# Kernel tuning notes

Hardware: AMD Instinct MI355X
Metric: run time of the kernel (lower is better)

## Reference

```python
import jax, jax.numpy as jnp
import numpy as np

LMAX = 2
C1 = 64; C2 = 64; COUT = 64
B = 4096
SUM_RDIM = sum(3**L for L in range(LMAX + 1))   # 13
FEAT1 = C1 * SUM_RDIM                            # 832
FEAT2 = C2 * SUM_RDIM


def _enumerate_paths(Lmax):
    paths = []
    for L1 in range(Lmax + 1):
        for L2 in range(Lmax + 1):
            for k in range(min(L1, L2) + 1):
                Lout = L1 + L2 - 2 * k
                if 0 <= Lout <= Lmax:
                    paths.append((L1, L2, Lout, k, False))
            if L1 >= 1 and L2 >= 1:
                for k in range(min(L1 - 1, L2 - 1) + 1):
                    Lout = L1 + L2 - 2 * k - 1
                    if 0 <= Lout <= Lmax:
                        paths.append((L1, L2, Lout, k, True))
    return paths

PATHS = _enumerate_paths(LMAX)   # 15 paths for Lmax=2


def _path_eq(L1, L2, k, use_eps):
    # Fused equation: W[c,a,b] contracted together with the delta/eps path einsum.
    letters = list('defghijklmnopqrstuvwxyz')  # a,b,c reserved for channels
    i_idx = letters[:L1]
    j_idx = letters[L1:L1 + L2]
    for r in range(k):  # delta: contract last k indices of A with last k of B
        j_idx[L2 - k + r] = i_idx[L1 - k + r]
    i_free = i_idx[:L1 - k]
    j_free = j_idx[:L2 - k]
    eps_sub = None
    if use_eps:  # consume last free index of each side via eps_{p i j}
        p = letters[L1 + L2]
        eps_sub = p + i_free[-1] + j_free[-1]
        i_free, j_free = i_free[:-1], j_free[:-1]
        out = i_free + j_free + [p]
    else:
        out = i_free + j_free
    terms = ['cab', '...a' + ''.join(i_idx), '...b' + ''.join(j_idx)]
    if eps_sub is not None:
        terms.append(eps_sub)
    return ','.join(terms) + '->...c' + ''.join(out)


def _epsilon():
    e = np.zeros((3, 3, 3), dtype=np.float32)
    e[0, 1, 2] = e[1, 2, 0] = e[2, 0, 1] = 1.0
    e[2, 1, 0] = e[1, 0, 2] = e[0, 2, 1] = -1.0
    return jnp.asarray(e)


def _split_by_rank(x, C, Lmax):
    batch = x.shape[:-1]
    out, idx = {}, 0
    for L in range(Lmax + 1):
        d = C * 3**L
        blk = x[..., idx:idx + d]
        idx += d
        out[L] = blk.reshape(*batch, C) if L == 0 else blk.reshape(*batch, C, *((3,) * L))
    return out


def setup_inputs() -> dict:
    key = jax.random.key(0)
    k1, k2, k3 = jax.random.split(key, 3)
    x1 = jax.random.normal(k1, (B, FEAT1), dtype=jnp.float32)
    x2 = jax.random.normal(k2, (B, FEAT2), dtype=jnp.float32)
    weight = jax.random.normal(k3, (len(PATHS) * COUT * C1 * C2,), dtype=jnp.float32) * 0.02
    return {"x1": x1, "x2": x2, "weight": weight}


def reference(x1, x2, weight):
    A = _split_by_rank(x1, C1, LMAX)
    Bt = _split_by_rank(x2, C2, LMAX)
    eps = _epsilon().astype(x1.dtype)
    batch = x1.shape[:-1]
    blocks = {L: jnp.zeros((*batch, COUT) + (3,) * L, dtype=x1.dtype) for L in range(LMAX + 1)}
    wsz = COUT * C1 * C2
    for n, (L1, L2, Lout, k, use_eps) in enumerate(PATHS):
        Wp = weight[n * wsz:(n + 1) * wsz].reshape(COUT, C1, C2)
        eq = _path_eq(L1, L2, k, use_eps)
        ops = (Wp, A[L1], Bt[L2]) + ((eps,) if use_eps else ())
        blocks[Lout] = blocks[Lout] + jnp.einsum(eq, *ops, optimize='optimal')
    parts = [blocks[L].reshape(*batch, COUT * 3**L) for L in range(LMAX + 1)]
    return jnp.concatenate(parts, axis=-1)
```

## Files before the change

kernel.cpp:

```cpp
#include <hip/hip_runtime.h>
#include <cstdint>
#include <cstddef>


#define FEAT 832
#define ZT 64

typedef _Float16 half8 __attribute__((ext_vector_type(8)));
typedef float floatx16 __attribute__((ext_vector_type(16)));

struct Chunk {
  int wbase;
  int o1[3];
  int o2[3];
  float sg[3];
  int d1, d2, nt;
};

__global__ void swz_w_kernel(const float* __restrict__ w, _Float16* __restrict__ o) {
  const int i = blockIdx.x * 256 + threadIdx.x;
  const int lane = i & 63;
  const int pkc  = i >> 6;
  const int cgrp = pkc & 1;
  const int ksg  = (pkc >> 1) & 255;
  const int p    = pkc >> 9;
  const int c  = cgrp * 32 + (lane & 31);
  const int k0 = ksg * 16 + (lane >> 5) * 8;
  const float* src = w + (size_t)p * 262144 + (size_t)c * 4096 + k0;
  const float4 v0 = *(const float4*)(src);
  const float4 v1 = *(const float4*)(src + 4);
  half8 h = { (_Float16)v0.x, (_Float16)v0.y, (_Float16)v0.z, (_Float16)v0.w,
              (_Float16)v1.x, (_Float16)v1.y, (_Float16)v1.z, (_Float16)v1.w };
  *(half8*)(o + (size_t)i * 8) = h;
}

__global__ __launch_bounds__(256) void gather_kernel(
    float* __restrict__ out, const float* __restrict__ part, int np)
{
  __shared__ float T[64][65];
  const int zb = blockIdx.x * 64;
  const int fb = blockIdx.y * 64;
  const int tid = threadIdx.x;
  const int fl = tid >> 6;
  const int zl = tid & 63;
  #pragma unroll
  for (int i = 0; i < 16; ++i) {
    const int f = fb + fl + i * 4;
    int s, c;
    if (f < 64)       { s = 0;              c = f; }
    else if (f < 256) { const int g = f - 64;  c = g / 3; s = 1 + g % 3; }
    else              { const int g = f - 256; c = g / 9; s = 4 + g % 9; }
    const size_t base = (size_t)s * 262144 + (size_t)c * 4096 + zb + zl;
    float v = 0.0f;
    for (int q = 0; q < np; ++q)
      v += part[(size_t)q * 3407872 + base];
    T[fl + i * 4][zl] = v;
  }
  __syncthreads();
  const int zr = tid >> 6;
  const int fc = tid & 63;
  #pragma unroll
  for (int i = 0; i < 16; ++i) {
    const int z = zr + i * 4;
    float* o = out + (size_t)(zb + z) * FEAT + fb + fc;
    *o += T[fc][z];
  }
}

__device__ __forceinline__ half8 splat8(_Float16 h) {
  return half8{h, h, h, h, h, h, h, h};
}

template<int NT>
__device__ __forceinline__ void run_chunk(
    const Chunk C, const int zbase, const int zl, const int hf,
    const int lane, const int tid,
    const float* __restrict__ x1, const float* __restrict__ x2,
    const _Float16* __restrict__ Wh,
    _Float16* __restrict__ XS2, _Float16* __restrict__ XS1,
    floatx16& acc0, floatx16& acc1)
{
  __syncthreads();

  #pragma unroll
  for (int t = 0; t < NT; ++t) {
    const size_t base2 = (size_t)zbase * FEAT + C.o2[t];
    for (int e = tid; e < 4096; e += 128) {
      const int zz = e >> 6, b = e & 63;
      XS2[(t * 64 + zz) * 72 + b] =
          (_Float16)x2[base2 + (size_t)zz * FEAT + b * C.d2];
    }
  }
  #pragma unroll
  for (int t = 0; t < NT; ++t) {
    const float sgf = C.sg[t];
    const int o1 = C.o1[t];
    for (int e = tid; e < 4096; e += 128) {
      const int a = e & 63, zz = e >> 6;
      XS1[(t * 64 + a) * 66 + zz] =
          (_Float16)(x1[(size_t)(zbase + zz) * FEAT + o1 + a * C.d1] * sgf);
    }
  }
  __syncthreads();

  half8 x2r[NT][4];
  #pragma unroll
  for (int t = 0; t < NT; ++t) {
    #pragma unroll
    for (int ks = 0; ks < 4; ++ks)
      x2r[t][ks] = *(const half8*)&XS2[(t * 64 + zl) * 72 + ks * 16 + hf * 8];
  }

  const _Float16* __restrict__ Wq = Wh + C.wbase + lane * 8;
  const _Float16* __restrict__ Xq = XS1 + zl;

  half8 afE[2][4], afO[2][4];
  #pragma unroll
  for (int ks = 0; ks < 4; ++ks) {
    afE[0][ks] = *(const half8*)(Wq + ks * 1024);
    afE[1][ks] = *(const half8*)(Wq + ks * 1024 + 512);
    afO[0][ks] = *(const half8*)(Wq + 4096 + ks * 1024);
    afO[1][ks] = *(const half8*)(Wq + 4096 + ks * 1024 + 512);
  }
  _Float16 sc[NT], scn[NT];
  #pragma unroll
  for (int t = 0; t < NT; ++t) {
    sc[t]  = Xq[(t * 64 + 0) * 66];
    scn[t] = Xq[(t * 64 + 1) * 66];
  }

  #pragma unroll 1
  for (int a = 0; a < 64; a += 2) {
    {
      half8 sv[NT];
      #pragma unroll
      for (int t = 0; t < NT; ++t) sv[t] = splat8(sc[t]);
      if (a + 2 < 64) {
        #pragma unroll
        for (int t = 0; t < NT; ++t) sc[t] = Xq[(t * 64 + a + 2) * 66];
      }
      #pragma unroll
      for (int ks = 0; ks < 4; ++ks) {
        half8 tb = sv[0] * x2r[0][ks];
        if (NT > 1) tb += sv[1] * x2r[1][ks];
        if (NT > 2) tb += sv[2] * x2r[2][ks];
        acc0 = __builtin_amdgcn_mfma_f32_32x32x16_f16(afE[0][ks], tb, acc0, 0, 0, 0);
        acc1 = __builtin_amdgcn_mfma_f32_32x32x16_f16(afE[1][ks], tb, acc1, 0, 0, 0);
      }
      if (a + 2 < 64) {
        const _Float16* wn = Wq + (a + 2) * 4096;
        #pragma unroll
        for (int ks = 0; ks < 4; ++ks) {
          afE[0][ks] = *(const half8*)(wn + ks * 1024);
          afE[1][ks] = *(const half8*)(wn + ks * 1024 + 512);
        }
      }
    }
    {
      half8 sv[NT];
      #pragma unroll
      for (int t = 0; t < NT; ++t) sv[t] = splat8(scn[t]);
      if (a + 3 < 64) {
        #pragma unroll
        for (int t = 0; t < NT; ++t) scn[t] = Xq[(t * 64 + a + 3) * 66];
      }
      #pragma unroll
      for (int ks = 0; ks < 4; ++ks) {
        half8 tb = sv[0] * x2r[0][ks];
        if (NT > 1) tb += sv[1] * x2r[1][ks];
        if (NT > 2) tb += sv[2] * x2r[2][ks];
        acc0 = __builtin_amdgcn_mfma_f32_32x32x16_f16(afO[0][ks], tb, acc0, 0, 0, 0);
        acc1 = __builtin_amdgcn_mfma_f32_32x32x16_f16(afO[1][ks], tb, acc1, 0, 0, 0);
      }
      if (a + 3 < 64) {
        const _Float16* wn = Wq + (a + 3) * 4096;
        #pragma unroll
        for (int ks = 0; ks < 4; ++ks) {
          afO[0][ks] = *(const half8*)(wn + ks * 1024);
          afO[1][ks] = *(const half8*)(wn + ks * 1024 + 512);
        }
      }
    }
  }
}

__global__ __launch_bounds__(128, 2) void tp_kernel(
    const float* __restrict__ x1, const float* __restrict__ x2,
    const _Float16* __restrict__ Wh, float* __restrict__ out,
    float* __restrict__ part)
{
  __shared__ __align__(16) _Float16 XS2[3 * 64 * 72];
  __shared__ __align__(16) _Float16 XS1[3 * 64 * 66];
  __shared__ Chunk chs[7];
  __shared__ int nch_s;

  const int tid  = threadIdx.x;
  const int slot = blockIdx.y;
  const int q    = blockIdx.z;
  const int nsplit = gridDim.z;
  const int zbase = blockIdx.x * ZT;
  const int zgrp = tid >> 6;
  const int lane = tid & 63;
  const int ln31 = lane & 31;
  const int hf   = lane >> 5;
  const int zl   = zgrp * 32 + ln31;

  int offO, dO, mO;
  if (slot == 0)      { offO = 0;   dO = 1; mO = 0; }
  else if (slot < 4)  { offO = 64;  dO = 3; mO = slot - 1; }
  else                { offO = 256; dO = 9; mO = slot - 4; }

  if (tid == 0) {
    int n = 0;
    auto add = [&](int p, int L1, int L2,
                   int i0, int i1, int i2, int j0, int j1, int j2,
                   float s0, float s1, float s2, int nt) {
      const int offs[3] = {0, 64, 256};
      const int ds[3]   = {1, 3, 9};
      Chunk c;
      c.wbase = p * 262144;
      c.o1[0] = offs[L1] + i0; c.o1[1] = offs[L1] + i1; c.o1[2] = offs[L1] + i2;
      c.o2[0] = offs[L2] + j0; c.o2[1] = offs[L2] + j1; c.o2[2] = offs[L2] + j2;
      c.sg[0] = s0; c.sg[1] = s1; c.sg[2] = s2;
      c.d1 = ds[L1]; c.d2 = ds[L2]; c.nt = nt;
      chs[n++] = c;
    };
    if (slot == 0) {
      add(0, 0,0, 0,0,0, 0,0,0, 1,0,0, 1);
      add(5, 1,1, 0,1,2, 0,1,2, 1,1,1, 3);
      add(13,2,2, 0,1,2, 0,1,2, 1,1,1, 3);
      add(13,2,2, 3,4,5, 3,4,5, 1,1,1, 3);
      add(13,2,2, 6,7,8, 6,7,8, 1,1,1, 3);
    } else if (slot < 4) {
      const int m = slot - 1, p1 = (m+1)%3, p2 = (m+2)%3;
      add(1, 0,1, 0,0,0, m,0,0, 1,0,0, 1);
      add(3, 1,0, m,0,0, 0,0,0, 1,0,0, 1);
      add(6, 1,1, p1,p2,0, p2,p1,0, 1,-1,0, 2);
      add(7, 1,2, 0,1,2, 3*m,3*m+1,3*m+2, 1,1,1, 3);
      add(10,2,1, 3*m,3*m+1,3*m+2, 0,1,2, 1,1,1, 3);
      add(14,2,2, 3*p1,3*p1+1,3*p1+2, 3*p2,3*p2+1,3*p2+2, 1,1,1, 3);
      add(14,2,2, 3*p2,3*p2+1,3*p2+2, 3*p1,3*p1+1,3*p1+2, -1,-1,-1, 3);
    } else {
      const int m = slot - 4, u = m/3, v = m%3, q1 = (v+1)%3, q2 = (v+2)%3;
      add(2, 0,2, 0,0,0, m,0,0, 1,0,0, 1);
      add(4, 1,1, u,0,0, v,0,0, 1,0,0, 1);
      add(8, 1,2, q1,q2,0, 3*u+q2,3*u+q1,0, 1,-1,0, 2);
      add(9, 2,0, m,0,0, 0,0,0, 1,0,0, 1);
      add(11,2,1, 3*u+q1,3*u+q2,0, q2,q1,0, 1,-1,0, 2);
      add(12,2,2, 3*u,3*u+1,3*u+2, 3*v,3*v+1,3*v+2, 1,1,1, 3);
    }
    nch_s = n;
  }
  __syncthreads();
  const int nch = nch_s;

  floatx16 acc0, acc1;
  #pragma unroll
  for (int r = 0; r < 16; ++r) { acc0[r] = 0.0f; acc1[r] = 0.0f; }

  for (int ci = q; ci < nch; ci += nsplit) {
    const Chunk C = chs[ci];
    if (C.nt == 1)      run_chunk<1>(C, zbase, zl, hf, lane, tid, x1, x2, Wh, XS2, XS1, acc0, acc1);
    else if (C.nt == 2) run_chunk<2>(C, zbase, zl, hf, lane, tid, x1, x2, Wh, XS2, XS1, acc0, acc1);
    else                run_chunk<3>(C, zbase, zl, hf, lane, tid, x1, x2, Wh, XS2, XS1, acc0, acc1);
  }

  if (q == 0) {
    float* __restrict__ op = out + (size_t)(zbase + zl) * FEAT + offO + mO;
    #pragma unroll
    for (int r = 0; r < 16; ++r) {
      const int cr = (r & 3) + 8 * (r >> 2) + 4 * hf;
      op[(size_t)cr * dO]        = acc0[r];
      op[(size_t)(cr + 32) * dO] = acc1[r];
    }
  } else {
    float* __restrict__ op = part + (size_t)(q - 1) * 3407872
                                  + (size_t)slot * 262144 + (zbase + zl);
    #pragma unroll
    for (int r = 0; r < 16; ++r) {
      const int cr = (r & 3) + 8 * (r >> 2) + 4 * hf;
      op[(size_t)cr * 4096]        = acc0[r];
      op[(size_t)(cr + 32) * 4096] = acc1[r];
    }
  }
}

extern "C" void kernel_launch(void* const* d_in, const int* in_sizes, int n_in,
                              void* d_out, int out_size, void* d_ws, size_t ws_size,
                              hipStream_t stream) {
  const float* x1 = (const float*)d_in[0];
  const float* x2 = (const float*)d_in[1];
  const float* w  = (const float*)d_in[2];
  float* out = (float*)d_out;
  _Float16* Wh = (_Float16*)d_ws;
  float* part = (float*)((char*)d_ws + 7864320);

  const size_t plane_bytes = 3407872ull * 4ull;
  int np = (ws_size > 7864320) ? (int)((ws_size - 7864320) / plane_bytes) : 1;
  if (np > 3) np = 3;
  if (np < 1) np = 1;
  const int nsplit = np + 1;

  const int nchunks = 15 * 64 * 4096 / 8;
  hipLaunchKernelGGL(swz_w_kernel, dim3(nchunks / 256), dim3(256), 0, stream, w, Wh);

  dim3 grid(64, 13, nsplit);
  hipLaunchKernelGGL(tp_kernel, grid, dim3(128), 0, stream, x1, x2, Wh, out, part);

  dim3 ggrid(64, 13);
  hipLaunchKernelGGL(gather_kernel, ggrid, dim3(256), 0, stream, out, part, np);
}
```

Measured before the change: 387.0 us.

## Split reduction over input channel across two extra waves per block

```diff
diff --git a/kernel.cpp b/kernel.cpp
--- a/kernel.cpp
+++ b/kernel.cpp
@@ -74,7 +74,7 @@
 template<int NT>
 __device__ __forceinline__ void run_chunk(
     const Chunk C, const int zbase, const int zl, const int hf,
-    const int lane, const int tid,
+    const int lane, const int tid, const int a0,
     const float* __restrict__ x1, const float* __restrict__ x2,
     const _Float16* __restrict__ Wh,
     _Float16* __restrict__ XS2, _Float16* __restrict__ XS1,
@@ -85,7 +85,7 @@
   #pragma unroll
   for (int t = 0; t < NT; ++t) {
     const size_t base2 = (size_t)zbase * FEAT + C.o2[t];
-    for (int e = tid; e < 4096; e += 128) {
+    for (int e = tid; e < 4096; e += 256) {
       const int zz = e >> 6, b = e & 63;
       XS2[(t * 64 + zz) * 72 + b] =
           (_Float16)x2[base2 + (size_t)zz * FEAT + b * C.d2];
@@ -95,7 +95,7 @@
   for (int t = 0; t < NT; ++t) {
     const float sgf = C.sg[t];
     const int o1 = C.o1[t];
-    for (int e = tid; e < 4096; e += 128) {
+    for (int e = tid; e < 4096; e += 256) {
       const int a = e & 63, zz = e >> 6;
       XS1[(t * 64 + a) * 66 + zz] =
           (_Float16)(x1[(size_t)(zbase + zz) * FEAT + o1 + a * C.d1] * sgf);
@@ -115,27 +115,29 @@
   const _Float16* __restrict__ Xq = XS1 + zl;
 
   half8 afE[2][4], afO[2][4];
+  const _Float16* __restrict__ w0 = Wq + (size_t)a0 * 4096;
   #pragma unroll
   for (int ks = 0; ks < 4; ++ks) {
-    afE[0][ks] = *(const half8*)(Wq + ks * 1024);
-    afE[1][ks] = *(const half8*)(Wq + ks * 1024 + 512);
-    afO[0][ks] = *(const half8*)(Wq + 4096 + ks * 1024);
-    afO[1][ks] = *(const half8*)(Wq + 4096 + ks * 1024 + 512);
+    afE[0][ks] = *(const half8*)(w0 + ks * 1024);
+    afE[1][ks] = *(const half8*)(w0 + ks * 1024 + 512);
+    afO[0][ks] = *(const half8*)(w0 + 4096 + ks * 1024);
+    afO[1][ks] = *(const half8*)(w0 + 4096 + ks * 1024 + 512);
   }
   _Float16 sc[NT], scn[NT];
   #pragma unroll
   for (int t = 0; t < NT; ++t) {
-    sc[t]  = Xq[(t * 64 + 0) * 66];
-    scn[t] = Xq[(t * 64 + 1) * 66];
-  }
-
+    sc[t]  = Xq[(t * 64 + a0) * 66];
+    scn[t] = Xq[(t * 64 + a0 + 1) * 66];
+  }
+
+  const int aend = a0 + 32;
   #pragma unroll 1
-  for (int a = 0; a < 64; a += 2) {
+  for (int a = a0; a < aend; a += 2) {
     {
       half8 sv[NT];
       #pragma unroll
       for (int t = 0; t < NT; ++t) sv[t] = splat8(sc[t]);
-      if (a + 2 < 64) {
+      if (a + 2 < aend) {
         #pragma unroll
         for (int t = 0; t < NT; ++t) sc[t] = Xq[(t * 64 + a + 2) * 66];
       }
@@ -147,8 +149,8 @@
         acc0 = __builtin_amdgcn_mfma_f32_32x32x16_f16(afE[0][ks], tb, acc0, 0, 0, 0);
         acc1 = __builtin_amdgcn_mfma_f32_32x32x16_f16(afE[1][ks], tb, acc1, 0, 0, 0);
       }
-      if (a + 2 < 64) {
-        const _Float16* wn = Wq + (a + 2) * 4096;
+      if (a + 2 < aend) {
+        const _Float16* wn = Wq + (size_t)(a + 2) * 4096;
         #pragma unroll
         for (int ks = 0; ks < 4; ++ks) {
           afE[0][ks] = *(const half8*)(wn + ks * 1024);
@@ -160,7 +162,7 @@
       half8 sv[NT];
       #pragma unroll
       for (int t = 0; t < NT; ++t) sv[t] = splat8(scn[t]);
-      if (a + 3 < 64) {
+      if (a + 3 < aend) {
         #pragma unroll
         for (int t = 0; t < NT; ++t) scn[t] = Xq[(t * 64 + a + 3) * 66];
       }
@@ -172,8 +174,8 @@
         acc0 = __builtin_amdgcn_mfma_f32_32x32x16_f16(afO[0][ks], tb, acc0, 0, 0, 0);
         acc1 = __builtin_amdgcn_mfma_f32_32x32x16_f16(afO[1][ks], tb, acc1, 0, 0, 0);
       }
-      if (a + 3 < 64) {
-        const _Float16* wn = Wq + (a + 3) * 4096;
+      if (a + 3 < aend) {
+        const _Float16* wn = Wq + (size_t)(a + 3) * 4096;
         #pragma unroll
         for (int ks = 0; ks < 4; ++ks) {
           afO[0][ks] = *(const half8*)(wn + ks * 1024);
@@ -184,7 +186,7 @@
   }
 }
 
-__global__ __launch_bounds__(128, 2) void tp_kernel(
+__global__ __launch_bounds__(256, 3) void tp_kernel(
     const float* __restrict__ x1, const float* __restrict__ x2,
     const _Float16* __restrict__ Wh, float* __restrict__ out,
     float* __restrict__ part)
@@ -199,7 +201,10 @@
   const int q    = blockIdx.z;
   const int nsplit = gridDim.z;
   const int zbase = blockIdx.x * ZT;
-  const int zgrp = tid >> 6;
+  const int wid  = tid >> 6;
+  const int zgrp = wid & 1;
+  const int ah   = wid >> 1;
+  const int a0   = ah * 32;
   const int lane = tid & 63;
   const int ln31 = lane & 31;
   const int hf   = lane >> 5;
@@ -260,27 +265,45 @@
 
   for (int ci = q; ci < nch; ci += nsplit) {
     const Chunk C = chs[ci];
-    if (C.nt == 1)      run_chunk<1>(C, zbase, zl, hf, lane, tid, x1, x2, Wh, XS2, XS1, acc0, acc1);
-    else if (C.nt == 2) run_chunk<2>(C, zbase, zl, hf, lane, tid, x1, x2, Wh, XS2, XS1, acc0, acc1);
-    else                run_chunk<3>(C, zbase, zl, hf, lane, tid, x1, x2, Wh, XS2, XS1, acc0, acc1);
-  }
-
-  if (q == 0) {
-    float* __restrict__ op = out + (size_t)(zbase + zl) * FEAT + offO + mO;
+    if (C.nt == 1)      run_chunk<1>(C, zbase, zl, hf, lane, tid, a0, x1, x2, Wh, XS2, XS1, acc0, acc1);
+    else if (C.nt == 2) run_chunk<2>(C, zbase, zl, hf, lane, tid, a0, x1, x2, Wh, XS2, XS1, acc0, acc1);
+    else                run_chunk<3>(C, zbase, zl, hf, lane, tid, a0, x1, x2, Wh, XS2, XS1, acc0, acc1);
+  }
+
+  __syncthreads();
+  float* R = (float*)XS2;
+  if (ah == 1) {
     #pragma unroll
     for (int r = 0; r < 16; ++r) {
-      const int cr = (r & 3) + 8 * (r >> 2) + 4 * hf;
-      op[(size_t)cr * dO]        = acc0[r];
-      op[(size_t)(cr + 32) * dO] = acc1[r];
-    }
-  } else {
-    float* __restrict__ op = part + (size_t)(q - 1) * 3407872
-                                  + (size_t)slot * 262144 + (zbase + zl);
+      R[r * 128 + zgrp * 64 + lane]        = acc0[r];
+      R[(16 + r) * 128 + zgrp * 64 + lane] = acc1[r];
+    }
+  }
+  __syncthreads();
+  if (ah == 0) {
     #pragma unroll
     for (int r = 0; r < 16; ++r) {
-      const int cr = (r & 3) + 8 * (r >> 2) + 4 * hf;
-      op[(size_t)cr * 4096]        = acc0[r];
-      op[(size_t)(cr + 32) * 4096] = acc1[r];
+      acc0[r] += R[r * 128 + zgrp * 64 + lane];
+      acc1[r] += R[(16 + r) * 128 + zgrp * 64 + lane];
+    }
+
+    if (q == 0) {
+      float* __restrict__ op = out + (size_t)(zbase + zl) * FEAT + offO + mO;
+      #pragma unroll
+      for (int r = 0; r < 16; ++r) {
+        const int cr = (r & 3) + 8 * (r >> 2) + 4 * hf;
+        op[(size_t)cr * dO]        = acc0[r];
+        op[(size_t)(cr + 32) * dO] = acc1[r];
+      }
+    } else {
+      float* __restrict__ op = part + (size_t)(q - 1) * 3407872
+                                    + (size_t)slot * 262144 + (zbase + zl);
+      #pragma unroll
+      for (int r = 0; r < 16; ++r) {
+        const int cr = (r & 3) + 8 * (r >> 2) + 4 * hf;
+        op[(size_t)cr * 4096]        = acc0[r];
+        op[(size_t)(cr + 32) * 4096] = acc1[r];
+      }
     }
   }
 }
@@ -305,7 +328,7 @@
   hipLaunchKernelGGL(swz_w_kernel, dim3(nchunks / 256), dim3(256), 0, stream, w, Wh);
 
   dim3 grid(64, 13, nsplit);
-  hipLaunchKernelGGL(tp_kernel, grid, dim3(128), 0, stream, x1, x2, Wh, out, part);
+  hipLaunchKernelGGL(tp_kernel, grid, dim3(256), 0, stream, x1, x2, Wh, out, part);
 
   dim3 ggrid(64, 13);
   hipLaunchKernelGGL(gather_kernel, ggrid, dim3(256), 0, stream, out, part, np);
```

After: 721.2 us. +86.4%, slower.
